# Kernel optimization log

Measured on AMD Instinct MI355X. Metric: run time of the kernel, lower is better.

## Reference

```python
import jax, jax.numpy as jnp
import numpy as np

DIM = 1024
H = 16
HD = DIM // H          # head_dim = 64
SCALE = HD ** -0.5
LAMBDA_INIT = 0.1


def setup_inputs() -> dict:
    key = jax.random.key(0)
    ks = jax.random.split(key, 8)
    B, NQ, NKV = 4, 1024, 1024
    # xavier_uniform for linear weights; stored as (in, out) for x @ W
    def xavier(k, fan_in, fan_out):
        a = float(np.sqrt(6.0 / (fan_in + fan_out)))
        return jax.random.uniform(k, (fan_in, fan_out), jnp.float32, -a, a)
    return {
        "DriftData": jax.random.normal(ks[0], (B, NQ, DIM), jnp.float32),
        "OceanData": jax.random.normal(ks[1], (B, NKV, DIM), jnp.float32),
        "Wq": xavier(ks[2], DIM, 2 * DIM),
        "Wk": xavier(ks[3], DIM, 2 * DIM),
        "Wv": xavier(ks[4], DIM, DIM),
        "Wo": xavier(ks[5], DIM, DIM),
        "lambda_q1": jax.random.normal(ks[6], (H, HD), jnp.float32),
        "lambda_k1": jax.random.normal(jax.random.fold_in(ks[6], 1), (H, HD), jnp.float32),
        "lambda_q2": jax.random.normal(ks[7], (H, HD), jnp.float32),
        "lambda_k2": jax.random.normal(jax.random.fold_in(ks[7], 1), (H, HD), jnp.float32),
    }


def reference(DriftData, OceanData, Wq, Wk, Wv, Wo,
              lambda_q1, lambda_k1, lambda_q2, lambda_k2):
    B, NQ, dim = DriftData.shape
    NKV = OceanData.shape[1]
    # lambda scalar per head: exp(q1.k1) - exp(q2.k2) + lambda_init  -> (H,)
    lam = (jnp.exp(jnp.sum(lambda_q1 * lambda_k1, axis=-1))
           - jnp.exp(jnp.sum(lambda_q2 * lambda_k2, axis=-1)) + LAMBDA_INIT)
    # projections: Q,K -> 2*dim, V -> dim
    Q = (DriftData @ Wq).reshape(B, NQ, H, 2 * HD).transpose(0, 2, 1, 3)   # b h q 2hd
    K = (OceanData @ Wk).reshape(B, NKV, H, 2 * HD).transpose(0, 2, 1, 3)  # b h k 2hd
    V = (OceanData @ Wv).reshape(B, NKV, H, HD).transpose(0, 2, 1, 3)      # b h k hd
    Q1, Q2 = Q[..., :HD], Q[..., HD:]
    K1, K2 = K[..., :HD], K[..., HD:]
    A1 = jnp.einsum('bhqd,bhkd->bhqk', Q1, K1) * SCALE
    A2 = jnp.einsum('bhqd,bhkd->bhqk', Q2, K2) * SCALE
    att = jax.nn.softmax(A1, axis=-1) - lam[None, :, None, None] * jax.nn.softmax(A2, axis=-1)
    out = jnp.einsum('bhqk,bhkd->bhqd', att, V)            # b h q hd
    out = out.transpose(0, 2, 1, 3).reshape(B, NQ, dim)    # b q dim
    return out @ Wo
```

## Files before the change

kernel.cpp:

```cpp
#include <hip/hip_runtime.h>
#include <hip/hip_bf16.h>

typedef unsigned short u16;
typedef unsigned int u32;
typedef __attribute__((ext_vector_type(8))) short short8;
typedef __attribute__((ext_vector_type(4))) float f32x4;
typedef __attribute__((ext_vector_type(4))) u16 us4;

#define MFMA16(a,b,c) __builtin_amdgcn_mfma_f32_16x16x32_bf16(a,b,c,0,0,0)

__device__ __forceinline__ u16 f2b(float x){
  u32 u = __builtin_bit_cast(u32, x);
  u32 r = (u + 0x7fffu + ((u >> 16) & 1u)) >> 16;
  return (u16)r;
}
__device__ __forceinline__ u16 f2b_hw(float x){
  return __builtin_bit_cast(u16, __float2bfloat16(x));
}
__device__ __forceinline__ float ex2(float x){ return __builtin_amdgcn_exp2f(x); }

__device__ __forceinline__ void gll16(const u16* g, u16* l){
  __builtin_amdgcn_global_load_lds((const __attribute__((address_space(1))) u32*)g,
                                   (__attribute__((address_space(3))) u32*)l, 16, 0, 0);
}

__global__ __launch_bounds__(256) void k_conv2(const float* __restrict__ a, const float* __restrict__ bsrc,
                                               u16* __restrict__ ya, u16* __restrict__ yb){
  int bid = blockIdx.x;
  const float* x = (bid < 4096) ? a : bsrc;
  u16* y = (bid < 4096) ? ya : yb;
  int i = (bid & 4095) * 256 + threadIdx.x;
  float4 v = reinterpret_cast<const float4*>(x)[i];
  us4 o; o.x = f2b(v.x); o.y = f2b(v.y); o.z = f2b(v.z); o.w = f2b(v.w);
  reinterpret_cast<us4*>(y)[i] = o;
}

__global__ __launch_bounds__(256) void k_prep_w(const float* __restrict__ Wq, const float* __restrict__ Wk,
                                                const float* __restrict__ Wv, const float* __restrict__ Wo,
                                                u16* __restrict__ WqT, u16* __restrict__ WkvT,
                                                u16* __restrict__ WoT,
                                                const float* __restrict__ lq1, const float* __restrict__ lk1,
                                                const float* __restrict__ lq2, const float* __restrict__ lk2,
                                                float* __restrict__ lam){
  __shared__ float t[32][33];
  const int z = blockIdx.z;
  const float* W; u16* WT; int N; float scale = 1.0f;
  if (z == 0){ W = Wq; WT = WqT; N = 2048; scale = 0.1803368867f; }
  else if (z == 1){ W = Wk; WT = WkvT; N = 2048; }
  else if (z == 2){ W = Wv; WT = WkvT + 2048*1024; N = 1024; }
  else { W = Wo; WT = WoT; N = 1024; }
  int n0 = blockIdx.x * 32, k0 = blockIdx.y * 32;
  int tx = threadIdx.x & 31, ty = threadIdx.x >> 5;
  if (n0 < N){
    #pragma unroll
    for (int i = 0; i < 4; i++)
      t[ty + i*8][tx] = W[(size_t)(k0 + ty + i*8) * N + n0 + tx];
    __syncthreads();
    #pragma unroll
    for (int i = 0; i < 4; i++)
      WT[(size_t)(n0 + ty + i*8) * 1024 + k0 + tx] = f2b(t[tx][ty + i*8] * scale);
  }
  if (z == 3 && blockIdx.x == 0 && blockIdx.y == 0 && threadIdx.x < 16){
    int h = threadIdx.x;
    float d1 = 0.f, d2 = 0.f;
    for (int i = 0; i < 64; i++){
      d1 += lq1[h*64 + i] * lk1[h*64 + i];
      d2 += lq2[h*64 + i] * lk2[h*64 + i];
    }
    lam[h] = expf(d1) - expf(d2) + 0.1f;
  }
}

__global__ __launch_bounds__(256) void k_transpose_v(const u16* __restrict__ KV, u16* __restrict__ VT){
  __shared__ u16 t[32][34];
  int kv0 = blockIdx.x * 32, d0 = blockIdx.y * 32, bh = blockIdx.z;
  int b = bh >> 4, h = bh & 15;
  int tx = threadIdx.x & 31, ty = threadIdx.x >> 5;
  #pragma unroll
  for (int i = 0; i < 4; i++)
    t[ty + i*8][tx] = KV[(size_t)(b*1024 + kv0 + ty + i*8) * 3072 + 2048 + h*64 + d0 + tx];
  __syncthreads();
  #pragma unroll
  for (int i = 0; i < 4; i++)
    VT[(size_t)bh * 65536 + (size_t)(d0 + ty + i*8) * 1024 + kv0 + tx] = t[tx][ty + i*8];
}

template<bool OUTF32>
__device__ __forceinline__ void gemm_body(const u16* __restrict__ A, const u16* __restrict__ B,
                                          void* __restrict__ C, int N, int m0, int n0,
                                          u16* As, u16* Bs){
  const int tid = threadIdx.x;
  const int wave = tid >> 6, lane = tid & 63;
  const int lr = lane & 15, lg = lane >> 4;
  const int wm = wave >> 1, wn = wave & 1;

  f32x4 acc[4][4];
  #pragma unroll
  for (int i = 0; i < 4; i++)
    #pragma unroll
    for (int j = 0; j < 4; j++){ f32x4 z = {0.f,0.f,0.f,0.f}; acc[i][j] = z; }

  const int srow = tid >> 3;
  const int skc  = tid & 7;

  for (int k0 = 0; k0 < 1024; k0 += 64){
    #pragma unroll
    for (int c = 0; c < 4; c++){
      int row = c*32 + srow;
      const u16* ga = A + (size_t)(m0 + row) * 1024 + k0 + ((skc ^ (row & 7)) << 3);
      gll16(ga, As + c*2048 + wave*512);
      const u16* gb = B + (size_t)(n0 + row) * 1024 + k0 + ((skc ^ (row & 7)) << 3);
      gll16(gb, Bs + c*2048 + wave*512);
    }
    __syncthreads();
    #pragma unroll
    for (int kc = 0; kc < 2; kc++){
      short8 af[4], bfr[4];
      #pragma unroll
      for (int mt = 0; mt < 4; mt++){
        int row = wm*64 + mt*16 + lr;
        af[mt] = *reinterpret_cast<const short8*>(As + row*64 + (((kc*4 + lg) ^ (row & 7)) << 3));
      }
      #pragma unroll
      for (int nt = 0; nt < 4; nt++){
        int rown = wn*64 + nt*16 + lr;
        bfr[nt] = *reinterpret_cast<const short8*>(Bs + rown*64 + (((kc*4 + lg) ^ (rown & 7)) << 3));
      }
      #pragma unroll
      for (int mt = 0; mt < 4; mt++)
        #pragma unroll
        for (int nt = 0; nt < 4; nt++)
          acc[mt][nt] = MFMA16(af[mt], bfr[nt], acc[mt][nt]);
    }
    __syncthreads();
  }
  #pragma unroll
  for (int mt = 0; mt < 4; mt++)
    #pragma unroll
    for (int nt = 0; nt < 4; nt++)
      #pragma unroll
      for (int r = 0; r < 4; r++){
        int row = m0 + wm*64 + mt*16 + lg*4 + r;
        int col = n0 + wn*64 + nt*16 + lr;
        if (OUTF32) ((float*)C)[(size_t)row * N + col] = acc[mt][nt][r];
        else        ((u16*)C)[(size_t)row * N + col] = f2b(acc[mt][nt][r]);
      }
}

__global__ __launch_bounds__(256) void k_gemm_proj(const u16* __restrict__ Xd, const u16* __restrict__ Xo,
                                                   const u16* __restrict__ WqT, const u16* __restrict__ WkvT,
                                                   u16* __restrict__ Qb, u16* __restrict__ KVb){
  __shared__ __align__(16) u16 As[128*64];
  __shared__ __align__(16) u16 Bs[128*64];
  int bid0 = blockIdx.x;
  int bid = (bid0 & 7) * 160 + (bid0 >> 3);
  if (bid < 512){
    gemm_body<false>(Xd, WqT, Qb, 2048, (bid >> 4) * 128, (bid & 15) * 128, As, Bs);
  } else {
    int t = bid - 512;
    gemm_body<false>(Xo, WkvT, KVb, 3072, (t / 24) * 128, (t % 24) * 128, As, Bs);
  }
}

__global__ __launch_bounds__(256) void k_gemm_out(const u16* __restrict__ A, const u16* __restrict__ B,
                                                  float* __restrict__ C){
  __shared__ __align__(16) u16 As[128*64];
  __shared__ __align__(16) u16 Bs[128*64];
  int bid = blockIdx.x;
  gemm_body<true>(A, B, C, 1024, (bid >> 3) * 128, (bid & 7) * 128, As, Bs);
}

__device__ __forceinline__ void softmax_t(f32x4 s[4], float& l, u16* pl, int lr, int lg){
  float sum = 0.f;
  #pragma unroll
  for (int nt = 0; nt < 4; nt++)
    #pragma unroll
    for (int r = 0; r < 4; r++){
      float p = ex2(s[nt][r]);
      s[nt][r] = p;
      sum += p;
    }
  sum += __shfl_xor(sum, 16);
  sum += __shfl_xor(sum, 32);
  l += sum;
  char* base = (char*)pl + lr * 128;
  const int swz = (lr & 7) << 4;
  #pragma unroll
  for (int nt = 0; nt < 4; nt++){
    us4 h;
    h.x = f2b_hw(s[nt][0]); h.y = f2b_hw(s[nt][1]);
    h.z = f2b_hw(s[nt][2]); h.w = f2b_hw(s[nt][3]);
    *reinterpret_cast<us4*>(base + ((nt*32 + lg*8) ^ swz)) = h;
  }
}

__global__ __launch_bounds__(256, 2) void k_attn(const u16* __restrict__ Q, const u16* __restrict__ KVb,
                                                 const u16* __restrict__ VT, const float* __restrict__ lam,
                                                 u16* __restrict__ O){
  int bid = blockIdx.x;
  int logical = (bid & 7) * 64 + (bid >> 3);
  int qt8 = logical & 7, h = (logical >> 3) & 15, b = logical >> 7;
  const int tid = threadIdx.x, wave = tid >> 6, lane = tid & 63;
  const int lr = lane & 15, lg = lane >> 4;
  const int qb = qt8 * 128 + wave * 32;

  __shared__ __align__(16) u16 Ks[2][8192];
  __shared__ __align__(16) u16 Vs[2][4096];
  __shared__ __align__(16) u16 Pl[4][2][2][1024];

  const int srow = tid >> 4, schunk = tid & 15;
  const int vrow = tid >> 3, vchunk = tid & 7;
  const u16* Kg = KVb + (size_t)(b*1024 + srow) * 3072 + h*128 + ((schunk ^ (srow & 7)) << 3);
  const u16* Vg = VT + (size_t)(b*16 + h) * 65536 + (size_t)vrow * 1024 + ((vchunk ^ (vrow & 7)) << 3);

  short8 qf[2][2][2];
  #pragma unroll
  for (int qt = 0; qt < 2; qt++){
    const u16* Qp = Q + (size_t)(b*1024 + qb + qt*16 + lr) * 2048 + h*128 + lg*8;
    #pragma unroll
    for (int kc = 0; kc < 2; kc++){
      qf[0][qt][kc] = *reinterpret_cast<const short8*>(Qp + kc*32);
      qf[1][qt][kc] = *reinterpret_cast<const short8*>(Qp + 64 + kc*32);
    }
  }
  const float lamh = lam[h];

  f32x4 o[2][4][2];
  #pragma unroll
  for (int br = 0; br < 2; br++)
    #pragma unroll
    for (int nt = 0; nt < 4; nt++)
      #pragma unroll
      for (int qt = 0; qt < 2; qt++){ f32x4 z = {0.f,0.f,0.f,0.f}; o[br][nt][qt] = z; }
  float l[2][2] = {{0.f, 0.f}, {0.f, 0.f}};

  auto STAGE = [&](int buf, int kv0){
    u16* kd = &Ks[buf][tid * 8];
    #pragma unroll
    for (int i = 0; i < 4; i++)
      gll16(Kg + (size_t)(kv0 + i*16) * 3072, kd + i*2048);
    u16* vd = &Vs[buf][tid * 8];
    #pragma unroll
    for (int j = 0; j < 2; j++)
      gll16(Vg + kv0 + (size_t)(j*32) * 1024, vd + j*2048);
  };

  STAGE(0, 0);
  __syncthreads();

  for (int t = 0; t < 16; t++){
    const int cur = t & 1;
    if (t < 15) STAGE(cur ^ 1, (t + 1) << 6);

    const u16* kbuf = &Ks[cur][0];
    const u16* vbuf = &Vs[cur][0];

    #pragma unroll
    for (int br = 0; br < 2; br++){
      short8 kf[4][2];
      #pragma unroll
      for (int nt = 0; nt < 4; nt++)
        #pragma unroll
        for (int kc = 0; kc < 2; kc++)
          kf[nt][kc] = *reinterpret_cast<const short8*>(
              kbuf + (nt*16 + lr)*128 + (((br*8 + kc*4 + lg) ^ (lr & 7)) << 3));
      #pragma unroll
      for (int qt = 0; qt < 2; qt++){
        f32x4 s[4];
        #pragma unroll
        for (int nt = 0; nt < 4; nt++){ f32x4 z = {0.f,0.f,0.f,0.f}; s[nt] = z; }
        __builtin_amdgcn_s_setprio(1);
        #pragma unroll
        for (int nt = 0; nt < 4; nt++)
          #pragma unroll
          for (int kc = 0; kc < 2; kc++)
            s[nt] = MFMA16(kf[nt][kc], qf[br][qt][kc], s[nt]);
        __builtin_amdgcn_s_setprio(0);
        softmax_t(s, l[br][qt], &Pl[wave][qt][br][0], lr, lg);
      }
    }

    const int swz = (lr & 7) << 4;
    __builtin_amdgcn_s_setprio(1);
    #pragma unroll
    for (int kc = 0; kc < 2; kc++){
      short8 pf[2][2];
      #pragma unroll
      for (int qt = 0; qt < 2; qt++)
        #pragma unroll
        for (int br = 0; br < 2; br++)
          pf[qt][br] = *reinterpret_cast<const short8*>(
              (char*)&Pl[wave][qt][br][0] + lr*128 + ((kc*64 + lg*16) ^ swz));
      #pragma unroll
      for (int nt = 0; nt < 4; nt++){
        short8 vf = *reinterpret_cast<const short8*>(
            vbuf + (nt*16 + lr)*64 + (((kc*4 + lg) ^ (lr & 7)) << 3));
        #pragma unroll
        for (int qt = 0; qt < 2; qt++){
          o[0][nt][qt] = MFMA16(vf, pf[qt][0], o[0][nt][qt]);
          o[1][nt][qt] = MFMA16(vf, pf[qt][1], o[1][nt][qt]);
        }
      }
    }
    __builtin_amdgcn_s_setprio(0);
    __syncthreads();
  }

  #pragma unroll
  for (int qt = 0; qt < 2; qt++){
    const float inv1 = 1.0f / l[0][qt];
    const float inv2 = lamh / l[1][qt];
    u16* Op = O + (size_t)(b*1024 + qb + qt*16 + lr) * 1024 + h*64;
    #pragma unroll
    for (int nt = 0; nt < 4; nt++){
      us4 hh;
      #pragma unroll
      for (int r = 0; r < 4; r++){
        float v = o[0][nt][qt][r] * inv1 - o[1][nt][qt][r] * inv2;
        ((u16*)&hh)[r] = f2b_hw(v);
      }
      *reinterpret_cast<us4*>(Op + nt*16 + lg*4) = hh;
    }
  }
}

extern "C" void kernel_launch(void* const* d_in, const int* in_sizes, int n_in,
                              void* d_out, int out_size, void* d_ws, size_t ws_size,
                              hipStream_t stream){
  const float* Drift = (const float*)d_in[0];
  const float* Ocean = (const float*)d_in[1];
  const float* Wq    = (const float*)d_in[2];
  const float* Wk    = (const float*)d_in[3];
  const float* Wv    = (const float*)d_in[4];
  const float* Wo    = (const float*)d_in[5];
  const float* lq1   = (const float*)d_in[6];
  const float* lk1   = (const float*)d_in[7];
  const float* lq2   = (const float*)d_in[8];
  const float* lk2   = (const float*)d_in[9];
  float* out = (float*)d_out;

  char* ws = (char*)d_ws;
  u16* Xd   = (u16*)(ws);
  u16* Xo   = (u16*)(ws + 8388608);
  u16* WqT  = (u16*)(ws + 16777216);
  u16* WkvT = (u16*)(ws + 20971520);
  u16* WoT  = (u16*)(ws + 27262976);
  u16* Qb   = (u16*)(ws + 29360128);
  u16* KVb  = (u16*)(ws + 46137344);
  u16* VTb  = (u16*)(ws + 71303168);
  u16* Ob   = (u16*)(ws + 79691776);
  float* lam = (float*)(ws + 88080384);

  k_conv2<<<8192, 256, 0, stream>>>(Drift, Ocean, Xd, Xo);
  k_prep_w<<<dim3(64,32,4), 256, 0, stream>>>(Wq, Wk, Wv, Wo, WqT, WkvT, WoT,
                                              lq1, lk1, lq2, lk2, lam);
  k_gemm_proj<<<1280, 256, 0, stream>>>(Xd, Xo, WqT, WkvT, Qb, KVb);
  k_transpose_v<<<dim3(32,2,64), 256, 0, stream>>>(KVb, VTb);
  k_attn<<<512, 256, 0, stream>>>(Qb, KVb, VTb, lam, Ob);
  k_gemm_out<<<256, 256, 0, stream>>>(Ob, WoT, out);
}
```

Before: 144.5 us.

## Merge prep kernels, hoist GEMM address math, add occupancy hints, use hw bf16

Folds the activation conversion and weight transpose kernels into one launch of 16384 blocks, which saves one kernel launch. In the GEMM body, global and LDS addresses are now computed once before the k-loop and advanced by pointer increments instead of being recomputed on every iteration. The GEMM kernels get launch_bounds with a minimum of 4 blocks per CU, and the bf16 output conversion switches to the hardware intrinsic. The gains should be small and come mostly from fewer integer instructions and less launch overhead. The occupancy hint may push register spills.

```diff
diff --git a/kernel.cpp b/kernel.cpp
--- a/kernel.cpp
+++ b/kernel.cpp
@@ -24,32 +24,35 @@
                                    (__attribute__((address_space(3))) u32*)l, 16, 0, 0);
 }
 
-__global__ __launch_bounds__(256) void k_conv2(const float* __restrict__ a, const float* __restrict__ bsrc,
-                                               u16* __restrict__ ya, u16* __restrict__ yb){
+__global__ __launch_bounds__(256) void k_prep(const float* __restrict__ Drift, const float* __restrict__ Ocean,
+                                              const float* __restrict__ Wq, const float* __restrict__ Wk,
+                                              const float* __restrict__ Wv, const float* __restrict__ Wo,
+                                              u16* __restrict__ Xd, u16* __restrict__ Xo,
+                                              u16* __restrict__ WqT, u16* __restrict__ WkvT,
+                                              u16* __restrict__ WoT,
+                                              const float* __restrict__ lq1, const float* __restrict__ lk1,
+                                              const float* __restrict__ lq2, const float* __restrict__ lk2,
+                                              float* __restrict__ lam){
+  __shared__ float t[32][33];
   int bid = blockIdx.x;
-  const float* x = (bid < 4096) ? a : bsrc;
-  u16* y = (bid < 4096) ? ya : yb;
-  int i = (bid & 4095) * 256 + threadIdx.x;
-  float4 v = reinterpret_cast<const float4*>(x)[i];
-  us4 o; o.x = f2b(v.x); o.y = f2b(v.y); o.z = f2b(v.z); o.w = f2b(v.w);
-  reinterpret_cast<us4*>(y)[i] = o;
-}
-
-__global__ __launch_bounds__(256) void k_prep_w(const float* __restrict__ Wq, const float* __restrict__ Wk,
-                                                const float* __restrict__ Wv, const float* __restrict__ Wo,
-                                                u16* __restrict__ WqT, u16* __restrict__ WkvT,
-                                                u16* __restrict__ WoT,
-                                                const float* __restrict__ lq1, const float* __restrict__ lk1,
-                                                const float* __restrict__ lq2, const float* __restrict__ lk2,
-                                                float* __restrict__ lam){
-  __shared__ float t[32][33];
-  const int z = blockIdx.z;
+  if (bid < 8192){
+    const float* x = (bid < 4096) ? Drift : Ocean;
+    u16* y = (bid < 4096) ? Xd : Xo;
+    int i = (bid & 4095) * 256 + threadIdx.x;
+    float4 v = reinterpret_cast<const float4*>(x)[i];
+    us4 o; o.x = f2b(v.x); o.y = f2b(v.y); o.z = f2b(v.z); o.w = f2b(v.w);
+    reinterpret_cast<us4*>(y)[i] = o;
+    return;
+  }
+  int tt = bid - 8192;
+  int z = tt >> 11;
+  int bx = tt & 63, by = (tt & 2047) >> 6;
   const float* W; u16* WT; int N; float scale = 1.0f;
   if (z == 0){ W = Wq; WT = WqT; N = 2048; scale = 0.1803368867f; }
   else if (z == 1){ W = Wk; WT = WkvT; N = 2048; }
   else if (z == 2){ W = Wv; WT = WkvT + 2048*1024; N = 1024; }
   else { W = Wo; WT = WoT; N = 1024; }
-  int n0 = blockIdx.x * 32, k0 = blockIdx.y * 32;
+  int n0 = bx * 32, k0 = by * 32;
   int tx = threadIdx.x & 31, ty = threadIdx.x >> 5;
   if (n0 < N){
     #pragma unroll
@@ -60,7 +63,7 @@
     for (int i = 0; i < 4; i++)
       WT[(size_t)(n0 + ty + i*8) * 1024 + k0 + tx] = f2b(t[tx][ty + i*8] * scale);
   }
-  if (z == 3 && blockIdx.x == 0 && blockIdx.y == 0 && threadIdx.x < 16){
+  if (z == 3 && bx == 0 && by == 0 && threadIdx.x < 16){
     int h = threadIdx.x;
     float d1 = 0.f, d2 = 0.f;
     for (int i = 0; i < 64; i++){
@@ -93,6 +96,21 @@
   const int wave = tid >> 6, lane = tid & 63;
   const int lr = lane & 15, lg = lane >> 4;
   const int wm = wave >> 1, wn = wave & 1;
+  const int srow = tid >> 3, skc = tid & 7;
+
+  const u16* ga[4]; const u16* gb[4];
+  #pragma unroll
+  for (int c = 0; c < 4; c++){
+    int row = c*32 + srow;
+    int off = (skc ^ (row & 7)) << 3;
+    ga[c] = A + (size_t)(m0 + row) * 1024 + off;
+    gb[c] = B + (size_t)(n0 + row) * 1024 + off;
+  }
+  const int rba = (wm*64 + lr)*64, rbb = (wn*64 + lr)*64;
+  const u16* a0 = As + rba + (((0 + lg) ^ (lr & 7)) << 3);
+  const u16* a1 = As + rba + (((4 + lg) ^ (lr & 7)) << 3);
+  const u16* b0 = Bs + rbb + (((0 + lg) ^ (lr & 7)) << 3);
+  const u16* b1 = Bs + rbb + (((4 + lg) ^ (lr & 7)) << 3);
 
   f32x4 acc[4][4];
   #pragma unroll
@@ -100,32 +118,28 @@
     #pragma unroll
     for (int j = 0; j < 4; j++){ f32x4 z = {0.f,0.f,0.f,0.f}; acc[i][j] = z; }
 
-  const int srow = tid >> 3;
-  const int skc  = tid & 7;
-
-  for (int k0 = 0; k0 < 1024; k0 += 64){
+  u16* asd = As + wave*512;
+  u16* bsd = Bs + wave*512;
+
+  for (int t = 0; t < 16; t++){
     #pragma unroll
     for (int c = 0; c < 4; c++){
-      int row = c*32 + srow;
-      const u16* ga = A + (size_t)(m0 + row) * 1024 + k0 + ((skc ^ (row & 7)) << 3);
-      gll16(ga, As + c*2048 + wave*512);
-      const u16* gb = B + (size_t)(n0 + row) * 1024 + k0 + ((skc ^ (row & 7)) << 3);
-      gll16(gb, Bs + c*2048 + wave*512);
+      gll16(ga[c], asd + c*2048);
+      gll16(gb[c], bsd + c*2048);
+      ga[c] += 64; gb[c] += 64;
     }
     __syncthreads();
     #pragma unroll
     for (int kc = 0; kc < 2; kc++){
+      const u16* ab = kc ? a1 : a0;
+      const u16* bb = kc ? b1 : b0;
       short8 af[4], bfr[4];
       #pragma unroll
-      for (int mt = 0; mt < 4; mt++){
-        int row = wm*64 + mt*16 + lr;
-        af[mt] = *reinterpret_cast<const short8*>(As + row*64 + (((kc*4 + lg) ^ (row & 7)) << 3));
-      }
-      #pragma unroll
-      for (int nt = 0; nt < 4; nt++){
-        int rown = wn*64 + nt*16 + lr;
-        bfr[nt] = *reinterpret_cast<const short8*>(Bs + rown*64 + (((kc*4 + lg) ^ (rown & 7)) << 3));
-      }
+      for (int mt = 0; mt < 4; mt++)
+        af[mt] = *reinterpret_cast<const short8*>(ab + mt*1024);
+      #pragma unroll
+      for (int nt = 0; nt < 4; nt++)
+        bfr[nt] = *reinterpret_cast<const short8*>(bb + nt*1024);
       #pragma unroll
       for (int mt = 0; mt < 4; mt++)
         #pragma unroll
@@ -143,13 +157,13 @@
         int row = m0 + wm*64 + mt*16 + lg*4 + r;
         int col = n0 + wn*64 + nt*16 + lr;
         if (OUTF32) ((float*)C)[(size_t)row * N + col] = acc[mt][nt][r];
-        else        ((u16*)C)[(size_t)row * N + col] = f2b(acc[mt][nt][r]);
+        else        ((u16*)C)[(size_t)row * N + col] = f2b_hw(acc[mt][nt][r]);
       }
 }
 
-__global__ __launch_bounds__(256) void k_gemm_proj(const u16* __restrict__ Xd, const u16* __restrict__ Xo,
-                                                   const u16* __restrict__ WqT, const u16* __restrict__ WkvT,
-                                                   u16* __restrict__ Qb, u16* __restrict__ KVb){
+__global__ __launch_bounds__(256, 4) void k_gemm_proj(const u16* __restrict__ Xd, const u16* __restrict__ Xo,
+                                                      const u16* __restrict__ WqT, const u16* __restrict__ WkvT,
+                                                      u16* __restrict__ Qb, u16* __restrict__ KVb){
   __shared__ __align__(16) u16 As[128*64];
   __shared__ __align__(16) u16 Bs[128*64];
   int bid0 = blockIdx.x;
@@ -162,8 +176,8 @@
   }
 }
 
-__global__ __launch_bounds__(256) void k_gemm_out(const u16* __restrict__ A, const u16* __restrict__ B,
-                                                  float* __restrict__ C){
+__global__ __launch_bounds__(256, 4) void k_gemm_out(const u16* __restrict__ A, const u16* __restrict__ B,
+                                                     float* __restrict__ C){
   __shared__ __align__(16) u16 As[128*64];
   __shared__ __align__(16) u16 Bs[128*64];
   int bid = blockIdx.x;
@@ -351,9 +365,8 @@
   u16* Ob   = (u16*)(ws + 79691776);
   float* lam = (float*)(ws + 88080384);
 
-  k_conv2<<<8192, 256, 0, stream>>>(Drift, Ocean, Xd, Xo);
-  k_prep_w<<<dim3(64,32,4), 256, 0, stream>>>(Wq, Wk, Wv, Wo, WqT, WkvT, WoT,
-                                              lq1, lk1, lq2, lk2, lam);
+  k_prep<<<16384, 256, 0, stream>>>(Drift, Ocean, Wq, Wk, Wv, Wo, Xd, Xo,
+                                    WqT, WkvT, WoT, lq1, lk1, lq2, lk2, lam);
   k_gemm_proj<<<1280, 256, 0, stream>>>(Xd, Xo, WqT, WkvT, Qb, KVb);
   k_transpose_v<<<dim3(32,2,64), 256, 0, stream>>>(KVb, VTb);
   k_attn<<<512, 256, 0, stream>>>(Qb, KVb, VTb, lam, Ob);
```

Result: slower. 181.7 us (+25.8%).
